# Optimization experiments

Measured on AMD Instinct MI355X. Metric: run time of the kernel, lower is better.

The kernel has to match this reference:

```python
import jax, jax.numpy as jnp
import numpy as np

B, IN, NC, O, H = 256, 2048, 1000, 4096, 4  # batch, in_features, num_classes, n_decoders, hidden
NEG_SLOPE = 0.1

def setup_inputs() -> dict:
    key = jax.random.key(0)
    ks = jax.random.split(key, 7)
    s1 = 1.0 / np.sqrt(IN)
    s2 = 1.0 / np.sqrt(H)
    return {
        "x":   jax.random.normal(ks[0], (B, IN), jnp.float32),
        "fcW": jax.random.normal(ks[1], (NC, IN), jnp.float32) * s1,
        "fcb": jax.random.normal(ks[2], (NC,), jnp.float32) * s1,
        "W1":  jax.random.normal(ks[3], (O, IN, H), jnp.float32) * s1,
        "b1":  jax.random.normal(ks[4], (O, H), jnp.float32) * s1,
        "W2":  jax.random.normal(ks[5], (O, H), jnp.float32) * s2,
        "b2":  jax.random.normal(ks[6], (O,), jnp.float32) * s2,
    }

def reference(x, fcW, fcb, W1, b1, W2, b2):
    # fc head: x1 = x @ fcW^T + fcb  -> [B, NC]
    x1 = jnp.einsum("bi,ci->bc", x, fcW) + fcb
    # 4096 tiny MLPs batched into one grouped GEMM:
    # h = leaky_relu(x @ W1_o + b1_o) for each decoder o  -> [B, O, H]
    h = jnp.einsum("bi,oih->boh", x, W1) + b1
    h = jnp.where(h >= 0, h, NEG_SLOPE * h)
    # second layer (H->1) collapses to a weighted reduction -> [B, O]
    x2 = jnp.einsum("boh,oh->bo", h, W2) + b2
    return (x1, x2)
```

## Files before the change

### kernel.cpp

```cpp
#include <hip/hip_runtime.h>


typedef __bf16 bf16_t;
typedef __bf16 bf16x2v __attribute__((ext_vector_type(2)));
typedef __bf16 bf16x8 __attribute__((ext_vector_type(8)));
typedef float  f32x4  __attribute__((ext_vector_type(4)));
typedef float  f32x16 __attribute__((ext_vector_type(16)));

#define WS_REP_BYTES (1 << 20)

__device__ __forceinline__ int bslot(int n, int g) {
    return g ^ (n & 7) ^ (((n >> 3) & 3) << 1);
}

__global__ __launch_bounds__(256)
void pack_a(const float* __restrict__ x, char* __restrict__ ws)
{
    const int kt  = blockIdx.x & 31;
    const int rep = blockIdx.x >> 5;
    char* dst = ws + (size_t)rep * WS_REP_BYTES + (size_t)kt * 32768;
    const int tid = threadIdx.x;
    #pragma unroll
    for (int ii = 0; ii < 8; ++ii) {
        const int gi  = tid + 256 * ii;
        const int mr5 = gi >> 8, g = (gi >> 5) & 7, l = gi & 31;
        const float* sp = x + (size_t)(mr5 * 32 + l) * 2048 + kt * 64 + g * 8;
        f32x4 v0 = *(const f32x4*)sp, v1 = *(const f32x4*)(sp + 4);
        bf16x8 o;
        #pragma unroll
        for (int c = 0; c < 4; ++c) { o[c] = (bf16_t)v0[c]; o[4 + c] = (bf16_t)v1[c]; }
        *(bf16x8*)(dst + gi * 16) = o;
    }
}

__global__ __launch_bounds__(256, 3)
void fused_dual(const char* __restrict__ ws,
                const float* __restrict__ W1,
                const float* __restrict__ fcW,
                const float* __restrict__ fcb,
                const float* __restrict__ b1,
                const float* __restrict__ W2,
                const float* __restrict__ b2,
                float* __restrict__ out)
{
    __shared__ __align__(16) char lds[2][4096];

    const int tid  = threadIdx.x;
    const int lane = tid & 63, w = tid >> 6;
    const int l31  = lane & 31, half = lane >> 5;

    const int idx = blockIdx.x;
    const int wid = (idx & 7) * 68 + (idx >> 3);
    const bool is_fc = (wid >= 512);
    const int d   = wid;
    const int fcI = wid - 512;

    const char* aRep = ws + (size_t)((idx & 7) >> 1) * WS_REP_BYTES;
    const int aoff = w * 8192 + half * 512 + l31 * 16;

    const float* bSrc;
    int bStep;
    int dwo[4];
    int fcWoff = 0;
    if (is_fc) {
        const int n = tid >> 3, kg = tid & 7;
        int c = fcI * 32 + n; if (c > 999) c = 999;
        bSrc = fcW + (size_t)c * 2048 + kg * 8;
        bStep = 64;
        fcWoff = n * 128 + bslot(n, kg) * 16;
        #pragma unroll
        for (int h = 0; h < 4; ++h) dwo[h] = 0;
    } else {
        const int o = (tid >> 5) & 7, kg = (tid >> 2) & 7, kp = tid & 3;
        bSrc = W1 + (size_t)(d * 8 + o) * 8192 + (kg * 8 + kp * 2) * 4;
        bStep = 256;
        #pragma unroll
        for (int h = 0; h < 4; ++h) {
            const int n = 4 * o + h;
            dwo[h] = n * 128 + bslot(n, kg) * 16 + kp * 4;
        }
    }

    int bro[4];
    #pragma unroll
    for (int ks = 0; ks < 4; ++ks)
        bro[ks] = l31 * 128 + bslot(l31, ks * 2 + half) * 16;

    f32x16 acc[2];
    #pragma unroll
    for (int i = 0; i < 2; ++i)
        #pragma unroll
        for (int r = 0; r < 16; ++r) acc[i][r] = 0.f;

    bf16x8 aF0[8], aF1[8];
    f32x4  bR0[2], bR1[2];

    auto A_PF = [&](int kt, bf16x8* F) {
        const char* ap = aRep + (size_t)kt * 32768 + aoff;
        #pragma unroll
        for (int i = 0; i < 2; ++i)
            #pragma unroll
            for (int ks = 0; ks < 4; ++ks)
                F[i * 4 + ks] = *(const bf16x8*)(ap + i * 4096 + ks * 1024);
    };
    auto B_LOAD = [&](int kt, f32x4* R) {
        const float* p = bSrc + (size_t)kt * bStep;
        R[0] = *(const f32x4*)p;
        R[1] = *(const f32x4*)(p + 4);
    };
    auto B_WRITE = [&](const f32x4* R, char* lB) {
        if (is_fc) {
            bf16x8 v;
            #pragma unroll
            for (int j = 0; j < 4; ++j) { v[j] = (bf16_t)R[0][j]; v[4 + j] = (bf16_t)R[1][j]; }
            *(bf16x8*)(lB + fcWoff) = v;
        } else {
            #pragma unroll
            for (int h = 0; h < 4; ++h) {
                bf16x2v v;
                v[0] = (bf16_t)R[0][h];
                v[1] = (bf16_t)R[1][h];
                *(bf16x2v*)(lB + dwo[h]) = v;
            }
        }
    };
    auto MM = [&](const bf16x8* F, const char* lB) {
        #pragma unroll
        for (int ks = 0; ks < 4; ++ks) {
            bf16x8 bf = *(const bf16x8*)(lB + bro[ks]);
            #pragma unroll
            for (int i = 0; i < 2; ++i)
                acc[i] = __builtin_amdgcn_mfma_f32_32x32x16_bf16(F[i * 4 + ks], bf, acc[i], 0, 0, 0);
        }
    };

    B_LOAD(0, bR0);
    B_LOAD(1, bR1);
    A_PF(0, aF0);
    B_WRITE(bR0, lds[0]);
    asm volatile("s_waitcnt lgkmcnt(0)" ::: "memory");
    __builtin_amdgcn_s_barrier();
    asm volatile("" ::: "memory");

    for (int t2 = 0; t2 < 16; ++t2) {
        const int t = t2 * 2;
        {
            A_PF(t + 1, aF1);
            int kb = t + 2; if (kb > 31) kb = 31;
            B_LOAD(kb, bR0);
            MM(aF0, lds[0]);
            B_WRITE(bR1, lds[1]);
            asm volatile("s_waitcnt lgkmcnt(0)" ::: "memory");
            __builtin_amdgcn_s_barrier();
            asm volatile("" ::: "memory");
        }
        {
            int ka = t + 2; if (ka > 31) ka = 31;
            A_PF(ka, aF0);
            int kb = t + 3; if (kb > 31) kb = 31;
            B_LOAD(kb, bR1);
            MM(aF1, lds[1]);
            B_WRITE(bR0, lds[0]);
            asm volatile("s_waitcnt lgkmcnt(0)" ::: "memory");
            __builtin_amdgcn_s_barrier();
            asm volatile("" ::: "memory");
        }
    }

    if (is_fc) {
        const int c = fcI * 32 + l31;
        if (c < 1000) {
            const float bias = fcb[c];
            #pragma unroll
            for (int i = 0; i < 2; ++i)
            #pragma unroll
            for (int r = 0; r < 16; ++r) {
                const int m = w * 64 + i * 32 + (r & 3) + 8 * (r >> 2) + 4 * half;
                out[m * 1000 + c] = acc[i][r] + bias;
            }
        }
    } else {
        float* x2 = out + 256 * 1000;
        const int n_glob = d * 32 + l31;
        const float b1v = b1[n_glob], w2v = W2[n_glob];
        const float b2v = b2[n_glob >> 2];
        float* xs = (float*)lds;
        const int o8 = l31 >> 2;
        #pragma unroll
        for (int i = 0; i < 2; ++i)
        #pragma unroll
        for (int r = 0; r < 16; ++r) {
            float h = acc[i][r] + b1v;
            h = (h >= 0.f) ? h : 0.1f * h;
            float wv = h * w2v;
            wv += __shfl_xor(wv, 1, 64);
            wv += __shfl_xor(wv, 2, 64);
            if ((lane & 3) == 0) {
                const int row = w * 64 + i * 32 + (r & 3) + 8 * (r >> 2) + 4 * half;
                xs[row * 8 + o8] = wv + b2v;
            }
        }
        __syncthreads();
        #pragma unroll
        for (int j = 0; j < 2; ++j) {
            const int row = (tid >> 1) + j * 128, part = tid & 1;
            f32x4 v = *(const f32x4*)(xs + row * 8 + part * 4);
            *(f32x4*)(x2 + (size_t)row * 4096 + d * 8 + part * 4) = v;
        }
    }
}

extern "C" void kernel_launch(void* const* d_in, const int* in_sizes, int n_in,
                              void* d_out, int out_size, void* d_ws, size_t ws_size,
                              hipStream_t stream)
{
    (void)in_sizes; (void)n_in; (void)out_size; (void)ws_size;
    const float* x   = (const float*)d_in[0];
    const float* fcW = (const float*)d_in[1];
    const float* fcb = (const float*)d_in[2];
    const float* W1  = (const float*)d_in[3];
    const float* b1  = (const float*)d_in[4];
    const float* W2  = (const float*)d_in[5];
    const float* b2  = (const float*)d_in[6];
    char* ws = (char*)d_ws;
    pack_a<<<128, 256, 0, stream>>>(x, ws);
    fused_dual<<<544, 256, 0, stream>>>(ws, W1, fcW, fcb, b1, W2, b2, (float*)d_out);
}
```

Measured before the change: 238.2 us.

## Split decoder tiles across two row groups and double k-step per barrier

```diff
diff --git a/kernel.cpp b/kernel.cpp
--- a/kernel.cpp
+++ b/kernel.cpp
@@ -12,6 +12,11 @@
 __device__ __forceinline__ int bslot(int n, int g) {
     return g ^ (n & 7) ^ (((n >> 3) & 3) << 1);
 }
+
+#define BARRIER() do { \
+    asm volatile("s_waitcnt lgkmcnt(0)" ::: "memory"); \
+    __builtin_amdgcn_s_barrier(); \
+    asm volatile("" ::: "memory"); } while (0)
 
 __global__ __launch_bounds__(256)
 void pack_a(const float* __restrict__ x, char* __restrict__ ws)
@@ -33,7 +38,7 @@
     }
 }
 
-__global__ __launch_bounds__(256, 3)
+__global__ __launch_bounds__(256, 4)
 void fused_dual(const char* __restrict__ ws,
                 const float* __restrict__ W1,
                 const float* __restrict__ fcW,
@@ -43,169 +48,216 @@
                 const float* __restrict__ b2,
                 float* __restrict__ out)
 {
-    __shared__ __align__(16) char lds[2][4096];
+    __shared__ __align__(16) char lds[2][8192];
 
     const int tid  = threadIdx.x;
     const int lane = tid & 63, w = tid >> 6;
     const int l31  = lane & 31, half = lane >> 5;
 
     const int idx = blockIdx.x;
-    const int wid = (idx & 7) * 68 + (idx >> 3);
-    const bool is_fc = (wid >= 512);
-    const int d   = wid;
-    const int fcI = wid - 512;
+    const int wid = (idx & 7) * 132 + (idx >> 3);
+    const bool is_fc = (wid >= 1024);
+    const int d8 = wid >> 1, rg = wid & 1;
+    const int fcI = wid - 1024;
 
     const char* aRep = ws + (size_t)((idx & 7) >> 1) * WS_REP_BYTES;
-    const int aoff = w * 8192 + half * 512 + l31 * 16;
-
-    const float* bSrc;
-    int bStep;
-    int dwo[4];
-    int fcWoff = 0;
-    if (is_fc) {
-        const int n = tid >> 3, kg = tid & 7;
-        int c = fcI * 32 + n; if (c > 999) c = 999;
-        bSrc = fcW + (size_t)c * 2048 + kg * 8;
-        bStep = 64;
-        fcWoff = n * 128 + bslot(n, kg) * 16;
-        #pragma unroll
-        for (int h = 0; h < 4; ++h) dwo[h] = 0;
-    } else {
-        const int o = (tid >> 5) & 7, kg = (tid >> 2) & 7, kp = tid & 3;
-        bSrc = W1 + (size_t)(d * 8 + o) * 8192 + (kg * 8 + kp * 2) * 4;
-        bStep = 256;
-        #pragma unroll
-        for (int h = 0; h < 4; ++h) {
-            const int n = 4 * o + h;
-            dwo[h] = n * 128 + bslot(n, kg) * 16 + kp * 4;
-        }
-    }
 
     int bro[4];
     #pragma unroll
     for (int ks = 0; ks < 4; ++ks)
         bro[ks] = l31 * 128 + bslot(l31, ks * 2 + half) * 16;
 
-    f32x16 acc[2];
-    #pragma unroll
-    for (int i = 0; i < 2; ++i)
-        #pragma unroll
-        for (int r = 0; r < 16; ++r) acc[i][r] = 0.f;
-
-    bf16x8 aF0[8], aF1[8];
-    f32x4  bR0[2], bR1[2];
-
-    auto A_PF = [&](int kt, bf16x8* F) {
-        const char* ap = aRep + (size_t)kt * 32768 + aoff;
-        #pragma unroll
-        for (int i = 0; i < 2; ++i)
+    if (!is_fc) {
+        const int aoff = (rg * 4 + w) * 4096 + half * 512 + l31 * 16;
+        const int o = (tid >> 5) & 7, kg = (tid >> 2) & 7, kp = tid & 3;
+        const float* bSrc = W1 + (size_t)(d8 * 8 + o) * 8192 + (kg * 8 + kp * 2) * 4;
+        int dwo[4];
+        #pragma unroll
+        for (int h = 0; h < 4; ++h) {
+            const int n = 4 * o + h;
+            dwo[h] = n * 128 + bslot(n, kg) * 16 + kp * 4;
+        }
+
+        f32x16 acc;
+        #pragma unroll
+        for (int r = 0; r < 16; ++r) acc[r] = 0.f;
+
+        bf16x8 aF0[4], aF1[4];
+        f32x4  bRa[4], bRb[4];
+
+        auto B_LOAD = [&](int ss, f32x4* R) {
+            const float* p = bSrc + (size_t)ss * 512;
+            R[0] = *(const f32x4*)p;       R[1] = *(const f32x4*)(p + 4);
+            R[2] = *(const f32x4*)(p+256); R[3] = *(const f32x4*)(p + 260);
+        };
+        auto B_WRITE = [&](const f32x4* R, char* lB) {
+            #pragma unroll
+            for (int ktl = 0; ktl < 2; ++ktl)
+                #pragma unroll
+                for (int h = 0; h < 4; ++h) {
+                    bf16x2v v;
+                    v[0] = (bf16_t)R[ktl * 2][h];
+                    v[1] = (bf16_t)R[ktl * 2 + 1][h];
+                    *(bf16x2v*)(lB + ktl * 4096 + dwo[h]) = v;
+                }
+        };
+        auto A_PF = [&](int kt, bf16x8* F) {
+            const char* ap = aRep + (size_t)kt * 32768 + aoff;
             #pragma unroll
             for (int ks = 0; ks < 4; ++ks)
-                F[i * 4 + ks] = *(const bf16x8*)(ap + i * 4096 + ks * 1024);
-    };
-    auto B_LOAD = [&](int kt, f32x4* R) {
-        const float* p = bSrc + (size_t)kt * bStep;
-        R[0] = *(const f32x4*)p;
-        R[1] = *(const f32x4*)(p + 4);
-    };
-    auto B_WRITE = [&](const f32x4* R, char* lB) {
-        if (is_fc) {
-            bf16x8 v;
-            #pragma unroll
-            for (int j = 0; j < 4; ++j) { v[j] = (bf16_t)R[0][j]; v[4 + j] = (bf16_t)R[1][j]; }
-            *(bf16x8*)(lB + fcWoff) = v;
-        } else {
-            #pragma unroll
-            for (int h = 0; h < 4; ++h) {
-                bf16x2v v;
-                v[0] = (bf16_t)R[0][h];
-                v[1] = (bf16_t)R[1][h];
-                *(bf16x2v*)(lB + dwo[h]) = v;
-            }
-        }
-    };
-    auto MM = [&](const bf16x8* F, const char* lB) {
-        #pragma unroll
-        for (int ks = 0; ks < 4; ++ks) {
-            bf16x8 bf = *(const bf16x8*)(lB + bro[ks]);
-            #pragma unroll
-            for (int i = 0; i < 2; ++i)
-                acc[i] = __builtin_amdgcn_mfma_f32_32x32x16_bf16(F[i * 4 + ks], bf, acc[i], 0, 0, 0);
-        }
-    };
-
-    B_LOAD(0, bR0);
-    B_LOAD(1, bR1);
-    A_PF(0, aF0);
-    B_WRITE(bR0, lds[0]);
-    asm volatile("s_waitcnt lgkmcnt(0)" ::: "memory");
-    __builtin_amdgcn_s_barrier();
-    asm volatile("" ::: "memory");
-
-    for (int t2 = 0; t2 < 16; ++t2) {
-        const int t = t2 * 2;
-        {
-            A_PF(t + 1, aF1);
-            int kb = t + 2; if (kb > 31) kb = 31;
-            B_LOAD(kb, bR0);
-            MM(aF0, lds[0]);
-            B_WRITE(bR1, lds[1]);
-            asm volatile("s_waitcnt lgkmcnt(0)" ::: "memory");
-            __builtin_amdgcn_s_barrier();
-            asm volatile("" ::: "memory");
-        }
-        {
-            int ka = t + 2; if (ka > 31) ka = 31;
-            A_PF(ka, aF0);
-            int kb = t + 3; if (kb > 31) kb = 31;
-            B_LOAD(kb, bR1);
-            MM(aF1, lds[1]);
-            B_WRITE(bR0, lds[0]);
-            asm volatile("s_waitcnt lgkmcnt(0)" ::: "memory");
-            __builtin_amdgcn_s_barrier();
-            asm volatile("" ::: "memory");
-        }
-    }
-
-    if (is_fc) {
-        const int c = fcI * 32 + l31;
-        if (c < 1000) {
-            const float bias = fcb[c];
-            #pragma unroll
-            for (int i = 0; i < 2; ++i)
-            #pragma unroll
-            for (int r = 0; r < 16; ++r) {
-                const int m = w * 64 + i * 32 + (r & 3) + 8 * (r >> 2) + 4 * half;
-                out[m * 1000 + c] = acc[i][r] + bias;
-            }
-        }
-    } else {
+                F[ks] = *(const bf16x8*)(ap + ks * 1024);
+        };
+        auto MM = [&](const bf16x8* F, const char* lB, int ktl) {
+            #pragma unroll
+            for (int ks = 0; ks < 4; ++ks) {
+                bf16x8 bf = *(const bf16x8*)(lB + ktl * 4096 + bro[ks]);
+                acc = __builtin_amdgcn_mfma_f32_32x32x16_bf16(F[ks], bf, acc, 0, 0, 0);
+            }
+        };
+
+        B_LOAD(0, bRa); B_LOAD(1, bRb);
+        A_PF(0, aF0);
+        B_WRITE(bRa, lds[0]);
+        BARRIER();
+
+        #pragma unroll 1
+        for (int ss2 = 0; ss2 < 8; ++ss2) {
+            const int ss = ss2 * 2;
+            {
+                int sl = ss + 2; if (sl > 15) sl = 15;
+                B_LOAD(sl, bRa);
+                A_PF(2 * ss + 1, aF1);
+                MM(aF0, lds[0], 0);
+                int ka = 2 * ss + 2; if (ka > 31) ka = 31;
+                A_PF(ka, aF0);
+                MM(aF1, lds[0], 1);
+                B_WRITE(bRb, lds[1]);
+                BARRIER();
+            }
+            {
+                int sl = ss + 3; if (sl > 15) sl = 15;
+                B_LOAD(sl, bRb);
+                int ka = 2 * ss + 3; if (ka > 31) ka = 31;
+                A_PF(ka, aF1);
+                MM(aF0, lds[1], 0);
+                int kb = 2 * ss + 4; if (kb > 31) kb = 31;
+                A_PF(kb, aF0);
+                MM(aF1, lds[1], 1);
+                B_WRITE(bRa, lds[0]);
+                BARRIER();
+            }
+        }
+
         float* x2 = out + 256 * 1000;
-        const int n_glob = d * 32 + l31;
+        const int n_glob = d8 * 32 + l31;
         const float b1v = b1[n_glob], w2v = W2[n_glob];
         const float b2v = b2[n_glob >> 2];
         float* xs = (float*)lds;
         const int o8 = l31 >> 2;
         #pragma unroll
-        for (int i = 0; i < 2; ++i)
-        #pragma unroll
         for (int r = 0; r < 16; ++r) {
-            float h = acc[i][r] + b1v;
+            float h = acc[r] + b1v;
             h = (h >= 0.f) ? h : 0.1f * h;
             float wv = h * w2v;
             wv += __shfl_xor(wv, 1, 64);
             wv += __shfl_xor(wv, 2, 64);
             if ((lane & 3) == 0) {
-                const int row = w * 64 + i * 32 + (r & 3) + 8 * (r >> 2) + 4 * half;
+                const int row = w * 32 + (r & 3) + 8 * (r >> 2) + 4 * half;
                 xs[row * 8 + o8] = wv + b2v;
             }
         }
         __syncthreads();
-        #pragma unroll
-        for (int j = 0; j < 2; ++j) {
-            const int row = (tid >> 1) + j * 128, part = tid & 1;
+        {
+            const int row = tid >> 1, part = tid & 1;
             f32x4 v = *(const f32x4*)(xs + row * 8 + part * 4);
-            *(f32x4*)(x2 + (size_t)row * 4096 + d * 8 + part * 4) = v;
+            *(f32x4*)(x2 + (size_t)(rg * 128 + row) * 4096 + d8 * 8 + part * 4) = v;
+        }
+    } else {
+        const int aoff = w * 8192 + half * 512 + l31 * 16;
+        const int n = tid >> 3, kg = tid & 7;
+        int c = fcI * 32 + n; if (c > 999) c = 999;
+        const float* bSrc = fcW + (size_t)c * 2048 + kg * 8;
+        const int fcWoff = n * 128 + bslot(n, kg) * 16;
+
+        f32x16 acc[2];
+        #pragma unroll
+        for (int i = 0; i < 2; ++i)
+            #pragma unroll
+            for (int r = 0; r < 16; ++r) acc[i][r] = 0.f;
+
+        bf16x8 aF[8];
+        f32x4  bRa[4], bRb[4];
+
+        auto B_LOAD = [&](int ss, f32x4* R) {
+            const float* p = bSrc + (size_t)ss * 128;
+            R[0] = *(const f32x4*)p;        R[1] = *(const f32x4*)(p + 4);
+            R[2] = *(const f32x4*)(p + 64); R[3] = *(const f32x4*)(p + 68);
+        };
+        auto B_WRITE = [&](const f32x4* R, char* lB) {
+            #pragma unroll
+            for (int ktl = 0; ktl < 2; ++ktl) {
+                bf16x8 v;
+                #pragma unroll
+                for (int j = 0; j < 4; ++j) {
+                    v[j]     = (bf16_t)R[ktl * 2][j];
+                    v[4 + j] = (bf16_t)R[ktl * 2 + 1][j];
+                }
+                *(bf16x8*)(lB + ktl * 4096 + fcWoff) = v;
+            }
+        };
+        auto A_PF = [&](int kt) {
+            const char* ap = aRep + (size_t)kt * 32768 + aoff;
+            #pragma unroll
+            for (int i = 0; i < 2; ++i)
+                #pragma unroll
+                for (int ks = 0; ks < 4; ++ks)
+                    aF[i * 4 + ks] = *(const bf16x8*)(ap + i * 4096 + ks * 1024);
+        };
+        auto MM = [&](const char* lB, int ktl) {
+            #pragma unroll
+            for (int ks = 0; ks < 4; ++ks) {
+                bf16x8 bf = *(const bf16x8*)(lB + ktl * 4096 + bro[ks]);
+                #pragma unroll
+                for (int i = 0; i < 2; ++i)
+                    acc[i] = __builtin_amdgcn_mfma_f32_32x32x16_bf16(aF[i * 4 + ks], bf, acc[i], 0, 0, 0);
+            }
+        };
+
+        B_LOAD(0, bRa); B_LOAD(1, bRb);
+        B_WRITE(bRa, lds[0]);
+        BARRIER();
+
+        #pragma unroll 1
+        for (int ss2 = 0; ss2 < 8; ++ss2) {
+            const int ss = ss2 * 2;
+            {
+                int sl = ss + 2; if (sl > 15) sl = 15;
+                B_LOAD(sl, bRa);
+                A_PF(2 * ss);     MM(lds[0], 0);
+                A_PF(2 * ss + 1); MM(lds[0], 1);
+                B_WRITE(bRb, lds[1]);
+                BARRIER();
+            }
+            {
+                int sl = ss + 3; if (sl > 15) sl = 15;
+                B_LOAD(sl, bRb);
+                A_PF(2 * ss + 2); MM(lds[1], 0);
+                A_PF(2 * ss + 3); MM(lds[1], 1);
+                B_WRITE(bRa, lds[0]);
+                BARRIER();
+            }
+        }
+
+        const int cc = fcI * 32 + l31;
+        if (cc < 1000) {
+            const float bias = fcb[cc];
+            #pragma unroll
+            for (int i = 0; i < 2; ++i)
+            #pragma unroll
+            for (int r = 0; r < 16; ++r) {
+                const int m = w * 64 + i * 32 + (r & 3) + 8 * (r >> 2) + 4 * half;
+                out[m * 1000 + cc] = acc[i][r] + bias;
+            }
         }
     }
 }
@@ -224,5 +276,5 @@
     const float* b2  = (const float*)d_in[6];
     char* ws = (char*)d_ws;
     pack_a<<<128, 256, 0, stream>>>(x, ws);
-    fused_dual<<<544, 256, 0, stream>>>(ws, W1, fcW, fcb, b1, W2, b2, (float*)d_out);
-}
+    fused_dual<<<1056, 256, 0, stream>>>(ws, W1, fcW, fcb, b1, W2, b2, (float*)d_out);
+}
```

Result: slower. 247.6 us (+3.9%).

## Give each wave a private LDS B tile and drop block barriers from main loop

Applied to the files above, without the earlier changes.

```diff
diff --git a/kernel.cpp b/kernel.cpp
--- a/kernel.cpp
+++ b/kernel.cpp
@@ -2,7 +2,7 @@
 
 
 typedef __bf16 bf16_t;
-typedef __bf16 bf16x2v __attribute__((ext_vector_type(2)));
+typedef __bf16 bf16x4v __attribute__((ext_vector_type(4)));
 typedef __bf16 bf16x8 __attribute__((ext_vector_type(8)));
 typedef float  f32x4  __attribute__((ext_vector_type(4)));
 typedef float  f32x16 __attribute__((ext_vector_type(16)));
@@ -43,7 +43,7 @@
                 const float* __restrict__ b2,
                 float* __restrict__ out)
 {
-    __shared__ __align__(16) char lds[2][4096];
+    __shared__ __align__(16) char lds[4][8192];
 
     const int tid  = threadIdx.x;
     const int lane = tid & 63, w = tid >> 6;
@@ -56,35 +56,32 @@
     const int fcI = wid - 512;
 
     const char* aRep = ws + (size_t)((idx & 7) >> 1) * WS_REP_BYTES;
-    const int aoff = w * 8192 + half * 512 + l31 * 16;
-
-    const float* bSrc;
-    int bStep;
-    int dwo[4];
-    int fcWoff = 0;
+    char* myLds = lds[w];
+
+    const int aA0 = (2 * w) * 4096 + half * 512 + l31 * 16;
+
+    const int bro0 = l31 * 128 + bslot(l31, half) * 16;
+    const int bro1 = l31 * 128 + bslot(l31, 2 + half) * 16;
+
+    const float* bSrc; int bStep;
+    int dwo0 = 0, dwo1 = 0, dwo2 = 0, dwo3 = 0, fco0 = 0, fco1 = 0;
     if (is_fc) {
-        const int n = tid >> 3, kg = tid & 7;
+        const int n = lane >> 1, kh = lane & 1;
         int c = fcI * 32 + n; if (c > 999) c = 999;
-        bSrc = fcW + (size_t)c * 2048 + kg * 8;
-        bStep = 64;
-        fcWoff = n * 128 + bslot(n, kg) * 16;
-        #pragma unroll
-        for (int h = 0; h < 4; ++h) dwo[h] = 0;
+        bSrc = fcW + (size_t)c * 2048 + kh * 16;
+        bStep = 32;
+        fco0 = n * 128 + bslot(n, kh * 2) * 16;
+        fco1 = n * 128 + bslot(n, kh * 2 + 1) * 16;
     } else {
-        const int o = (tid >> 5) & 7, kg = (tid >> 2) & 7, kp = tid & 3;
-        bSrc = W1 + (size_t)(d * 8 + o) * 8192 + (kg * 8 + kp * 2) * 4;
-        bStep = 256;
-        #pragma unroll
-        for (int h = 0; h < 4; ++h) {
-            const int n = 4 * o + h;
-            dwo[h] = n * 128 + bslot(n, kg) * 16 + kp * 4;
-        }
-    }
-
-    int bro[4];
-    #pragma unroll
-    for (int ks = 0; ks < 4; ++ks)
-        bro[ks] = l31 * 128 + bslot(l31, ks * 2 + half) * 16;
+        const int o = lane >> 3, sub = lane & 7;
+        bSrc = W1 + (size_t)(d * 8 + o) * 8192 + sub * 16;
+        bStep = 128;
+        const int g0 = sub >> 1, h8 = (sub & 1) * 8;
+        dwo0 = (4 * o + 0) * 128 + bslot(4 * o + 0, g0) * 16 + h8;
+        dwo1 = (4 * o + 1) * 128 + bslot(4 * o + 1, g0) * 16 + h8;
+        dwo2 = (4 * o + 2) * 128 + bslot(4 * o + 2, g0) * 16 + h8;
+        dwo3 = (4 * o + 3) * 128 + bslot(4 * o + 3, g0) * 16 + h8;
+    }
 
     f32x16 acc[2];
     #pragma unroll
@@ -92,80 +89,79 @@
         #pragma unroll
         for (int r = 0; r < 16; ++r) acc[i][r] = 0.f;
 
-    bf16x8 aF0[8], aF1[8];
-    f32x4  bR0[2], bR1[2];
-
-    auto A_PF = [&](int kt, bf16x8* F) {
-        const char* ap = aRep + (size_t)kt * 32768 + aoff;
-        #pragma unroll
-        for (int i = 0; i < 2; ++i)
-            #pragma unroll
-            for (int ks = 0; ks < 4; ++ks)
-                F[i * 4 + ks] = *(const bf16x8*)(ap + i * 4096 + ks * 1024);
-    };
-    auto B_LOAD = [&](int kt, f32x4* R) {
-        const float* p = bSrc + (size_t)kt * bStep;
-        R[0] = *(const f32x4*)p;
-        R[1] = *(const f32x4*)(p + 4);
-    };
-    auto B_WRITE = [&](const f32x4* R, char* lB) {
+    f32x4  bA[4], bB[4];
+    bf16x8 fA[4], fB[4];
+
+    auto G_B = [&](int t, f32x4* R) {
+        if (t > 63) t = 63;
+        const float* p = bSrc + (size_t)t * bStep;
+        #pragma unroll
+        for (int j = 0; j < 4; ++j) R[j] = *(const f32x4*)(p + j * 4);
+    };
+    auto G_A = [&](int t, bf16x8* F) {
+        if (t > 63) t = 63;
+        const char* base = aRep + (size_t)(t >> 1) * 32768 + (t & 1) * 2048 + aA0;
+        F[0] = *(const bf16x8*)(base);
+        F[1] = *(const bf16x8*)(base + 4096);
+        F[2] = *(const bf16x8*)(base + 1024);
+        F[3] = *(const bf16x8*)(base + 4096 + 1024);
+    };
+    auto W_B = [&](int t, const f32x4* R) {
+        char* buf = myLds + (((t >> 1) & 1) << 12);
+        const int phx = (t & 1) << 6;
         if (is_fc) {
-            bf16x8 v;
-            #pragma unroll
-            for (int j = 0; j < 4; ++j) { v[j] = (bf16_t)R[0][j]; v[4 + j] = (bf16_t)R[1][j]; }
-            *(bf16x8*)(lB + fcWoff) = v;
+            bf16x8 v0, v1;
+            #pragma unroll
+            for (int j = 0; j < 4; ++j) {
+                v0[j] = (bf16_t)R[0][j]; v0[4 + j] = (bf16_t)R[1][j];
+                v1[j] = (bf16_t)R[2][j]; v1[4 + j] = (bf16_t)R[3][j];
+            }
+            *(bf16x8*)(buf + (fco0 ^ phx)) = v0;
+            *(bf16x8*)(buf + (fco1 ^ phx)) = v1;
         } else {
-            #pragma unroll
-            for (int h = 0; h < 4; ++h) {
-                bf16x2v v;
-                v[0] = (bf16_t)R[0][h];
-                v[1] = (bf16_t)R[1][h];
-                *(bf16x2v*)(lB + dwo[h]) = v;
-            }
-        }
-    };
-    auto MM = [&](const bf16x8* F, const char* lB) {
-        #pragma unroll
-        for (int ks = 0; ks < 4; ++ks) {
-            bf16x8 bf = *(const bf16x8*)(lB + bro[ks]);
-            #pragma unroll
-            for (int i = 0; i < 2; ++i)
-                acc[i] = __builtin_amdgcn_mfma_f32_32x32x16_bf16(F[i * 4 + ks], bf, acc[i], 0, 0, 0);
-        }
-    };
-
-    B_LOAD(0, bR0);
-    B_LOAD(1, bR1);
-    A_PF(0, aF0);
-    B_WRITE(bR0, lds[0]);
-    asm volatile("s_waitcnt lgkmcnt(0)" ::: "memory");
-    __builtin_amdgcn_s_barrier();
-    asm volatile("" ::: "memory");
-
-    for (int t2 = 0; t2 < 16; ++t2) {
-        const int t = t2 * 2;
-        {
-            A_PF(t + 1, aF1);
-            int kb = t + 2; if (kb > 31) kb = 31;
-            B_LOAD(kb, bR0);
-            MM(aF0, lds[0]);
-            B_WRITE(bR1, lds[1]);
-            asm volatile("s_waitcnt lgkmcnt(0)" ::: "memory");
-            __builtin_amdgcn_s_barrier();
-            asm volatile("" ::: "memory");
-        }
-        {
-            int ka = t + 2; if (ka > 31) ka = 31;
-            A_PF(ka, aF0);
-            int kb = t + 3; if (kb > 31) kb = 31;
-            B_LOAD(kb, bR1);
-            MM(aF1, lds[1]);
-            B_WRITE(bR0, lds[0]);
-            asm volatile("s_waitcnt lgkmcnt(0)" ::: "memory");
-            __builtin_amdgcn_s_barrier();
-            asm volatile("" ::: "memory");
-        }
-    }
+            bf16x4v v0, v1, v2, v3;
+            #pragma unroll
+            for (int j = 0; j < 4; ++j) {
+                v0[j] = (bf16_t)R[j][0]; v1[j] = (bf16_t)R[j][1];
+                v2[j] = (bf16_t)R[j][2]; v3[j] = (bf16_t)R[j][3];
+            }
+            *(bf16x4v*)(buf + (dwo0 ^ phx)) = v0;
+            *(bf16x4v*)(buf + (dwo1 ^ phx)) = v1;
+            *(bf16x4v*)(buf + (dwo2 ^ phx)) = v2;
+            *(bf16x4v*)(buf + (dwo3 ^ phx)) = v3;
+        }
+    };
+    auto MM = [&](int t, const bf16x8* F) {
+        const char* buf = myLds + (((t >> 1) & 1) << 12);
+        const int phx = (t & 1) << 6;
+        bf16x8 b0 = *(const bf16x8*)(buf + (bro0 ^ phx));
+        bf16x8 b1 = *(const bf16x8*)(buf + (bro1 ^ phx));
+        acc[0] = __builtin_amdgcn_mfma_f32_32x32x16_bf16(F[0], b0, acc[0], 0, 0, 0);
+        acc[1] = __builtin_amdgcn_mfma_f32_32x32x16_bf16(F[1], b0, acc[1], 0, 0, 0);
+        acc[0] = __builtin_amdgcn_mfma_f32_32x32x16_bf16(F[2], b1, acc[0], 0, 0, 0);
+        acc[1] = __builtin_amdgcn_mfma_f32_32x32x16_bf16(F[3], b1, acc[1], 0, 0, 0);
+    };
+
+    G_B(0, bA); G_B(1, bB); G_A(0, fA);
+    W_B(0, bA);
+    G_B(2, bA);
+
+    #pragma unroll 1
+    for (int s2 = 0; s2 < 32; ++s2) {
+        const int s = s2 * 2;
+        G_A(s + 1, fB);
+        MM(s, fA);
+        W_B(s + 1, bB);
+        G_B(s + 3, bB);
+        G_A(s + 2, fA);
+        MM(s + 1, fB);
+        if (s2 < 31) {
+            W_B(s + 2, bA);
+            G_B(s + 4, bA);
+        }
+    }
+
+    __syncthreads();
 
     if (is_fc) {
         const int c = fcI * 32 + l31;
```

Result: slower. 274.0 us (+15.0%).
